# Optimization experiments

Hardware: AMD Instinct MI355X
Metric: run time of the kernel (lower is better)

The kernel has to match this reference:

```python
import jax, jax.numpy as jnp
import numpy as np

D_MODEL = 256
D_EDGE = 64
EPS = 1e-05
INPUT_FEATS = 2 * D_MODEL + D_EDGE + 1  # 577


def _linear_params(key, fan_in, fan_out):
    k1, k2 = jax.random.split(key)
    lim = 1.0 / np.sqrt(fan_in)
    W = jax.random.uniform(k1, (fan_in, fan_out), minval=-lim, maxval=lim, dtype=jnp.float32)
    b = jax.random.uniform(k2, (fan_out,), minval=-lim, maxval=lim, dtype=jnp.float32)
    return W, b


def setup_inputs() -> dict:
    key = jax.random.key(0)
    ks = jax.random.split(key, 16)
    B, N = 8, 128
    inp = {
        "coords": jax.random.normal(ks[0], (B, N, 3), dtype=jnp.float32),
        "inv_feats": jax.random.normal(ks[1], (B, N, D_MODEL), dtype=jnp.float32),
        "adj_matrix": jnp.ones((B, N, N), dtype=jnp.float32),
        "atom_mask": jnp.ones((B, N), dtype=jnp.float32),
        "edge_feats": jax.random.normal(ks[2], (B, N, N, D_EDGE), dtype=jnp.float32),
    }
    inp["W_e1"], inp["b_e1"] = _linear_params(ks[3], INPUT_FEATS, D_MODEL)
    inp["W_e2"], inp["b_e2"] = _linear_params(ks[4], D_MODEL, D_MODEL)
    inp["W_att"], inp["b_att"] = _linear_params(ks[5], D_MODEL, 1)
    inp["W_h1"], inp["b_h1"] = _linear_params(ks[6], 2 * D_MODEL, D_MODEL)
    inp["W_h2"], inp["b_h2"] = _linear_params(ks[7], D_MODEL, D_MODEL)
    inp["W_x1"], inp["b_x1"] = _linear_params(ks[8], INPUT_FEATS, D_MODEL)
    inp["W_x2"], inp["b_x2"] = _linear_params(ks[9], D_MODEL, D_MODEL)
    inp["W_x3"], inp["b_x3"] = _linear_params(ks[10], D_MODEL, 1)
    return inp


def _pair_linear(W, b, node_feats, ef):
    # Linear over concat([node_i, node_j, ef]) without materializing the concat.
    # W: [2*d_model + d_edge + 1, out]
    d = D_MODEL
    hi = node_feats @ W[:d]          # [B,N,out]
    hj = node_feats @ W[d:2 * d]     # [B,N,out]
    he = ef @ W[2 * d:]              # [B,N,N,out]
    return hi[:, :, None, :] + hj[:, None, :, :] + he + b


def _egnn_forward(coords, inv_feats, adj_matrix, atom_mask, edge_feats,
                  W_e1, b_e1, W_e2, b_e2, W_att, b_att,
                  W_h1, b_h1, W_h2, b_h2, W_x1, b_x1, W_x2, b_x2, W_x3, b_x3):
    mask = atom_mask[..., None]                       # [B,N,1]
    diff = coords[:, :, None, :] - coords[:, None, :, :]   # [B,N,N,3]
    sq = jnp.sum(diff * diff, axis=-1, keepdims=True)      # [B,N,N,1]
    ef = jnp.concatenate([edge_feats, sq], axis=-1)        # [B,N,N,d_edge+1]
    adj = adj_matrix[..., None]                             # [B,N,N,1]

    # phi_e: Linear-SiLU-Linear-SiLU on pair features
    msg = jax.nn.silu(_pair_linear(W_e1, b_e1, inv_feats, ef))
    msg = jax.nn.silu(msg @ W_e2 + b_e2)                    # [B,N,N,d]

    att = jax.nn.sigmoid(msg @ W_att + b_att)               # [B,N,N,1]
    node_msg = jnp.sum(msg * att * adj, axis=2)             # [B,N,d]

    h = jnp.concatenate([inv_feats, node_msg], axis=-1)
    h = jax.nn.silu(h @ W_h1 + b_h1) @ W_h2 + b_h2          # [B,N,d]

    # phi_x: Linear-SiLU-Linear-SiLU-Linear -> scalar per edge
    ex = jax.nn.silu(_pair_linear(W_x1, b_x1, inv_feats, ef))
    ex = jax.nn.silu(ex @ W_x2 + b_x2)
    edge_attn = ex @ W_x3 + b_x3                             # [B,N,N,1]

    normalisers = jnp.sqrt(sq[..., 0] + EPS) + 1.0           # [B,N,N]
    weighted = diff * edge_attn / normalisers[..., None] * adj
    coord_updates = jnp.sum(weighted, axis=2)                # [B,N,3]
    num_nodes = jnp.sum(mask, axis=1) + 1.0                  # [B,1]
    coord_updates = coord_updates / num_nodes[:, :, None]

    out_coords = (coords + coord_updates) * mask
    out_feats = h * mask
    return out_coords, out_feats


def reference(coords, inv_feats, adj_matrix, atom_mask, edge_feats,
              W_e1, b_e1, W_e2, b_e2, W_att, b_att,
              W_h1, b_h1, W_h2, b_h2, W_x1, b_x1, W_x2, b_x2, W_x3, b_x3):
    return _egnn_forward(coords, inv_feats, adj_matrix, atom_mask, edge_feats,
                         W_e1, b_e1, W_e2, b_e2, W_att, b_att,
                         W_h1, b_h1, W_h2, b_h2, W_x1, b_x1, W_x2, b_x2, W_x3, b_x3)
```

## Files before the change

kernel.cpp:

```cpp
#include <hip/hip_runtime.h>

typedef __attribute__((ext_vector_type(8))) __bf16 bf16x8;
typedef __attribute__((ext_vector_type(4))) __bf16 bf16x4;
typedef __attribute__((ext_vector_type(4))) float f32x4;

__device__ __forceinline__ float fast_sig(float x) {
  return __builtin_amdgcn_rcpf(1.0f + __expf(-x));
}
__device__ __forceinline__ float siluf(float x) { return x * fast_sig(x); }
__device__ __forceinline__ __bf16 tobf(float x) { return (__bf16)x; }

__device__ __forceinline__ void stage16(const void* g, void* l) {
  __builtin_amdgcn_global_load_lds(
      (const __attribute__((address_space(1))) void*)g,
      (__attribute__((address_space(3))) void*)l, 16, 0, 0);
}

__device__ __forceinline__ void stage_slice(
    const __bf16* __restrict__ src, int ld, int off,
    __bf16* swbuf, int tid)
{
  const int w = tid >> 6;
  #pragma unroll
  for (int q = 0; q < 2; q++) {
    int t16 = q * 512 + tid;
    int c = t16 >> 2, slot = t16 & 3;
    int kpart = slot ^ ((c >> 1) & 3);
    const __bf16* g = src + (size_t)c * ld + off + kpart * 8;
    __bf16* l = swbuf + (size_t)(q * 512 + w * 64) * 8;
    stage16(g, l);
  }
}

__global__ __launch_bounds__(256) void k_prep(
    const float* __restrict__ We1, const float* __restrict__ Wx1,
    const float* __restrict__ We2, const float* __restrict__ Wx2,
    const float* __restrict__ Wh1, const float* __restrict__ Wh2,
    const float* __restrict__ invf,
    __bf16* __restrict__ wt_e, __bf16* __restrict__ wt_x,
    __bf16* __restrict__ w2e, __bf16* __restrict__ w2x,
    __bf16* __restrict__ wh1t, __bf16* __restrict__ wh2t,
    __bf16* __restrict__ hcat,
    float* __restrict__ nmsg, float* __restrict__ cupd)
{
  int idx = blockIdx.x * 256 + threadIdx.x;
  if (idx < 147456) {
    int kk = idx / 576, f = idx - kk * 576;
    wt_e[idx] = tobf(We1[f * 256 + kk]);
    wt_x[idx] = tobf(Wx1[f * 256 + kk]);
  }
  if (idx < 65536) {
    int c = idx >> 8, k = idx & 255;
    w2e[idx] = tobf(We2[k * 256 + c]);
    w2x[idx] = tobf(Wx2[k * 256 + c]);
    wh2t[idx] = tobf(Wh2[k * 256 + c]);
    f32x4 z = {0.f, 0.f, 0.f, 0.f};
    *(f32x4*)(nmsg + idx * 4) = z;
  }
  if (idx < 131072) {
    int c = idx >> 9, k = idx & 511;
    wh1t[idx] = tobf(Wh1[k * 256 + c]);
  }
  if (idx < 3072) cupd[idx] = 0.f;
  {
    int node = idx >> 8, k = idx & 255;
    hcat[node * 512 + k] = tobf(invf[idx]);
  }
}

template<int NKS>
__device__ __forceinline__ void node_gemm64(
    const __bf16* __restrict__ B, int ldb, int boff,
    const __bf16* __restrict__ A, int lda, int aoff,
    int row0, int tid, f32x4 acc[4][4])
{
  const int lane = tid & 63, wc = tid >> 6, lr = lane & 15, lg = lane >> 4;
  #pragma unroll
  for (int ks = 0; ks < NKS; ks++) {
    bf16x8 bB[4], aA[4];
    #pragma unroll
    for (int m = 0; m < 4; m++)
      bB[m] = *(const bf16x8*)(B + (size_t)(row0 + m * 16 + lr) * ldb + boff + ks * 32 + lg * 8);
    #pragma unroll
    for (int n = 0; n < 4; n++)
      aA[n] = *(const bf16x8*)(A + (size_t)(wc * 64 + n * 16 + lr) * lda + aoff + ks * 32 + lg * 8);
    #pragma unroll
    for (int m = 0; m < 4; m++)
      #pragma unroll
      for (int n = 0; n < 4; n++)
        acc[m][n] = __builtin_amdgcn_mfma_f32_16x16x32_bf16(aA[n], bB[m], acc[m][n], 0, 0, 0);
  }
}

__global__ __launch_bounds__(256) void k_nproj(
    const __bf16* __restrict__ hcat,
    const __bf16* __restrict__ wt_e, const __bf16* __restrict__ wt_x,
    const float* __restrict__ be1, const float* __restrict__ bx1,
    float* __restrict__ hie, float* __restrict__ hje,
    float* __restrict__ hix, float* __restrict__ hjx)
{
  const int tid = threadIdx.x;
  const int row0 = blockIdx.x * 64;
  const int mat = blockIdx.y;
  const __bf16* A = (mat < 2) ? wt_e : wt_x;
  const int aoff = (mat & 1) ? 256 : 0;
  const float* bias = (mat == 0) ? be1 : (mat == 2 ? bx1 : nullptr);
  float* out = (mat == 0) ? hie : (mat == 1) ? hje : (mat == 2) ? hix : hjx;

  f32x4 acc[4][4];
  #pragma unroll
  for (int m = 0; m < 4; m++)
    #pragma unroll
    for (int n = 0; n < 4; n++) { f32x4 z = {0.f,0.f,0.f,0.f}; acc[m][n] = z; }
  node_gemm64<8>(hcat, 512, 0, A, 576, aoff, row0, tid, acc);

  const int lane = tid & 63, wc = tid >> 6, lr = lane & 15, lg = lane >> 4;
  #pragma unroll
  for (int m = 0; m < 4; m++) {
    int node = row0 + m * 16 + lr;
    #pragma unroll
    for (int n = 0; n < 4; n++) {
      int c0 = wc * 64 + n * 16 + lg * 4;
      f32x4 v = acc[m][n];
      if (bias) v += *(const f32x4*)(bias + c0);
      *(f32x4*)(out + (size_t)node * 256 + c0) = v;
    }
  }
}

__global__ __launch_bounds__(256) void k_mid(
    const float* __restrict__ nmsg, __bf16* __restrict__ hcat)
{
  int idx = blockIdx.x * 256 + threadIdx.x;
  int node = idx >> 8, k = idx & 255;
  hcat[node * 512 + 256 + k] = tobf(nmsg[idx]);
}

__global__ __launch_bounds__(256) void k_h1(
    const __bf16* __restrict__ hcat, const __bf16* __restrict__ wh1t,
    const float* __restrict__ bh1, __bf16* __restrict__ h1b)
{
  const int tid = threadIdx.x;
  const int row0 = blockIdx.x * 64;
  f32x4 acc[4][4];
  #pragma unroll
  for (int m = 0; m < 4; m++)
    #pragma unroll
    for (int n = 0; n < 4; n++) { f32x4 z = {0.f,0.f,0.f,0.f}; acc[m][n] = z; }
  node_gemm64<16>(hcat, 512, 0, wh1t, 512, 0, row0, tid, acc);

  const int lane = tid & 63, wc = tid >> 6, lr = lane & 15, lg = lane >> 4;
  #pragma unroll
  for (int m = 0; m < 4; m++) {
    int node = row0 + m * 16 + lr;
    #pragma unroll
    for (int n = 0; n < 4; n++) {
      int c0 = wc * 64 + n * 16 + lg * 4;
      f32x4 b4 = *(const f32x4*)(bh1 + c0);
      bf16x4 pk;
      #pragma unroll
      for (int r = 0; r < 4; r++) pk[r] = tobf(siluf(acc[m][n][r] + b4[r]));
      *(bf16x4*)(h1b + (size_t)node * 256 + c0) = pk;
    }
  }
}

__global__ __launch_bounds__(256) void k_h2(
    const __bf16* __restrict__ h1b, const __bf16* __restrict__ wh2t,
    const float* __restrict__ bh2, const float* __restrict__ amask,
    const float* __restrict__ coords, const float* __restrict__ cupd,
    float* __restrict__ out_feats, float* __restrict__ out_coords)
{
  __shared__ float sM[2];
  const int tid = threadIdx.x;
  const int row0 = blockIdx.x * 64;
  const int b = row0 >> 7;
  f32x4 acc[4][4];
  #pragma unroll
  for (int m = 0; m < 4; m++)
    #pragma unroll
    for (int n = 0; n < 4; n++) { f32x4 z = {0.f,0.f,0.f,0.f}; acc[m][n] = z; }
  node_gemm64<8>(h1b, 256, 0, wh2t, 256, 0, row0, tid, acc);

  if (tid < 128) {
    float v = amask[b * 128 + tid];
    #pragma unroll
    for (int off = 1; off < 64; off <<= 1) v += __shfl_xor(v, off);
    if ((tid & 63) == 0) sM[tid >> 6] = v;
  }
  __syncthreads();
  const float sNum = sM[0] + sM[1];

  const int lane = tid & 63, wc = tid >> 6, lr = lane & 15, lg = lane >> 4;
  #pragma unroll
  for (int m = 0; m < 4; m++) {
    int node = row0 + m * 16 + lr;
    float msk = amask[node];
    #pragma unroll
    for (int n = 0; n < 4; n++) {
      int c0 = wc * 64 + n * 16 + lg * 4;
      f32x4 b4 = *(const f32x4*)(bh2 + c0);
      f32x4 v = (acc[m][n] + b4) * msk;
      *(f32x4*)(out_feats + (size_t)node * 256 + c0) = v;
    }
  }
  if (tid < 192) {
    int nl = tid / 3, d = tid - nl * 3;
    int node = row0 + nl;
    float upd = cupd[node * 3 + d] / (sNum + 1.0f);
    out_coords[node * 3 + d] = (coords[node * 3 + d] + upd) * amask[node];
  }
}

template<bool EPATH>
__device__ __forceinline__ void egnn_path(
    int tid, char* sSb, __bf16* sW0, __bf16* sW1,
    const float* shi, const float* slast, const float* sqv, const float* sAdj,
    const float* __restrict__ hjb,
    const __bf16* __restrict__ wt,
    const __bf16* __restrict__ w2,
    const float* __restrict__ bias2, const float* __restrict__ vvec,
    float* sRed, float batt0, float* sNM, float* sCup,
    const float* __restrict__ coords, int jg0,
    float cix, float ciy, float ciz, const bf16x8 bE[2][2])
{
  const int lane = tid & 63, w = tid >> 6;
  const int lr = lane & 15, lg = lane >> 4;
  const int cg = (w & 3) * 64;
  const int jw = (w >> 2) * 32;
  const int slot = lg ^ ((lr >> 1) & 3);
  const int awbase = (cg + lr) * 32 + slot * 8;

  stage_slice(wt, 576, 512, sW0, tid);

  f32x4 hjf[2][4];
  #pragma unroll
  for (int m = 0; m < 2; m++) {
    const int jl = jw + m * 16 + lr;
    #pragma unroll
    for (int n = 0; n < 4; n++)
      hjf[m][n] = *(const f32x4*)(hjb + (size_t)jl * 256 + cg + n * 16 + lg * 4);
  }

  f32x4 acc[2][4];
  #pragma unroll
  for (int m = 0; m < 2; m++)
    #pragma unroll
    for (int n = 0; n < 4; n++) { f32x4 z = {0.f,0.f,0.f,0.f}; acc[m][n] = z; }

  __syncthreads();

  stage_slice(wt, 576, 544, sW1, tid);
  {
    bf16x8 aW[4];
    #pragma unroll
    for (int n = 0; n < 4; n++) aW[n] = *(const bf16x8*)(sW0 + awbase + n * 512);
    #pragma unroll
    for (int m = 0; m < 2; m++)
      #pragma unroll
      for (int n = 0; n < 4; n++)
        acc[m][n] = __builtin_amdgcn_mfma_f32_16x16x32_bf16(aW[n], bE[0][m], acc[m][n], 0, 0, 0);
  }
  __syncthreads();

  stage_slice(w2, 256, 0, sW0, tid);
  {
    bf16x8 aW[4];
    #pragma unroll
    for (int n = 0; n < 4; n++) aW[n] = *(const bf16x8*)(sW1 + awbase + n * 512);
    #pragma unroll
    for (int m = 0; m < 2; m++)
      #pragma unroll
      for (int n = 0; n < 4; n++)
        acc[m][n] = __builtin_amdgcn_mfma_f32_16x16x32_bf16(aW[n], bE[1][m], acc[m][n], 0, 0, 0);
  }
  #pragma unroll
  for (int m = 0; m < 2; m++) {
    const int jl = jw + m * 16 + lr;
    const float sq = sqv[jl];
    #pragma unroll
    for (int n = 0; n < 4; n++) {
      const int kk0 = cg + n * 16 + lg * 4;
      f32x4 hi4 = *(const f32x4*)(shi + kk0);
      f32x4 sl4 = *(const f32x4*)(slast + kk0);
      bf16x4 pk;
      #pragma unroll
      for (int r = 0; r < 4; r++)
        pk[r] = tobf(siluf(acc[m][n][r] + hi4[r] + hjf[m][n][r] + sq * sl4[r]));
      int off = (jl * 512 + kk0 * 2) ^ ((jl & 7) << 4);
      *(bf16x4*)(sSb + off) = pk;
      f32x4 z = {0.f, 0.f, 0.f, 0.f};
      acc[m][n] = z;
    }
  }
  __syncthreads();

  #pragma unroll
  for (int ks = 0; ks < 8; ks++) {
    if (ks < 7)
      stage_slice(w2, 256, (ks + 1) * 32, (ks & 1) ? sW0 : sW1, tid);
    const __bf16* sw = (ks & 1) ? sW1 : sW0;
    bf16x8 aW[4], bS[2];
    #pragma unroll
    for (int m = 0; m < 2; m++) {
      const int jl = jw + m * 16 + lr;
      int off = (jl * 512 + (ks * 32 + lg * 8) * 2) ^ ((jl & 7) << 4);
      bS[m] = *(const bf16x8*)(sSb + off);
    }
    #pragma unroll
    for (int n = 0; n < 4; n++) aW[n] = *(const bf16x8*)(sw + awbase + n * 512);
    #pragma unroll
    for (int m = 0; m < 2; m++)
      #pragma unroll
      for (int n = 0; n < 4; n++)
        acc[m][n] = __builtin_amdgcn_mfma_f32_16x16x32_bf16(aW[n], bS[m], acc[m][n], 0, 0, 0);
    __syncthreads();
  }

  float p[2] = {0.f, 0.f};
  #pragma unroll
  for (int n = 0; n < 4; n++) {
    f32x4 bb = *(const f32x4*)(bias2 + cg + n * 16 + lg * 4);
    f32x4 vv = *(const f32x4*)(vvec  + cg + n * 16 + lg * 4);
    #pragma unroll
    for (int m = 0; m < 2; m++)
      #pragma unroll
      for (int r = 0; r < 4; r++) {
        float s = siluf(acc[m][n][r] + bb[r]);
        acc[m][n][r] = s;
        p[m] += s * vv[r];
      }
  }
  #pragma unroll
  for (int m = 0; m < 2; m++) {
    p[m] += __shfl_xor(p[m], 16);
    p[m] += __shfl_xor(p[m], 32);
  }
  if (lane < 16) {
    #pragma unroll
    for (int m = 0; m < 2; m++)
      atomicAdd(&sRed[jw + m * 16 + lr], p[m]);
  }
  __syncthreads();

  if constexpr (EPATH) {
    float aw[2];
    #pragma unroll
    for (int m = 0; m < 2; m++) {
      int jl = jw + m * 16 + lr;
      aw[m] = fast_sig(sRed[jl] + batt0) * sAdj[jl];
    }
    f32x4 q[4];
    #pragma unroll
    for (int n = 0; n < 4; n++) { f32x4 z = {0.f,0.f,0.f,0.f}; q[n] = z; }
    #pragma unroll
    for (int m = 0; m < 2; m++)
      #pragma unroll
      for (int n = 0; n < 4; n++)
        q[n] += acc[m][n] * aw[m];
    #pragma unroll
    for (int off = 1; off < 16; off <<= 1)
      #pragma unroll
      for (int n = 0; n < 4; n++)
        #pragma unroll
        for (int r = 0; r < 4; r++)
          q[n][r] += __shfl_xor(q[n][r], off);
    if (lr == 0) {
      #pragma unroll
      for (int n = 0; n < 4; n++)
        #pragma unroll
        for (int r = 0; r < 4; r++)
          atomicAdd(&sNM[cg + n * 16 + lg * 4 + r], q[n][r]);
    }
  } else {
    if (tid < 64) {
      int jl = tid;
      int jgl = jg0 + jl;
      float ea = sRed[jl] + batt0;
      float wgt = ea * __builtin_amdgcn_rcpf(sqrtf(sqv[jl] + 1e-5f) + 1.0f) * sAdj[jl];
      float wx = wgt * (cix - coords[jgl * 3 + 0]);
      float wy = wgt * (ciy - coords[jgl * 3 + 1]);
      float wz = wgt * (ciz - coords[jgl * 3 + 2]);
      #pragma unroll
      for (int off = 1; off < 64; off <<= 1) {
        wx += __shfl_xor(wx, off);
        wy += __shfl_xor(wy, off);
        wz += __shfl_xor(wz, off);
      }
      if (tid == 0) { sCup[0] = wx; sCup[1] = wy; sCup[2] = wz; }
    }
  }
}

__global__ __launch_bounds__(512, 4) void k_edge(
    const float* __restrict__ coords, const float* __restrict__ adjm,
    const float* __restrict__ ef,
    const float* __restrict__ We1, const float* __restrict__ Wx1,
    const float* __restrict__ batt,
    const float* __restrict__ be2, const float* __restrict__ bx2,
    const float* __restrict__ bx3,
    const float* __restrict__ Watt, const float* __restrict__ Wx3,
    const float* __restrict__ hie, const float* __restrict__ hje,
    const float* __restrict__ hix, const float* __restrict__ hjx,
    const __bf16* __restrict__ wt_e, const __bf16* __restrict__ wt_x,
    const __bf16* __restrict__ w2e, const __bf16* __restrict__ w2x,
    float* __restrict__ nmsg, float* __restrict__ cupd)
{
  __shared__ __align__(16) char sSb[64 * 512];
  __shared__ __align__(16) __bf16 sW[2][8192];
  __shared__ float shie[256], shix[256], slaste[256], slastx[256];
  __shared__ float sqv[64], sAdj[64], sRedE[64], sRedX[64], sNM[256], sCup[4];

  const int tid = threadIdx.x;
  const int bi = blockIdx.x >> 1;
  const int half = blockIdx.x & 1;
  const int b = bi >> 7;
  const int j0g = half * 64;
  const int jg0 = b * 128 + j0g;

  const int lane = tid & 63, w = tid >> 6;
  const int lr = lane & 15, lg = lane >> 4;
  const int jw = (w >> 2) * 32;

  const float cix = coords[bi * 3 + 0];
  const float ciy = coords[bi * 3 + 1];
  const float ciz = coords[bi * 3 + 2];

  if (tid < 64) sRedE[tid] = 0.f;
  else if (tid < 128) sRedX[tid - 64] = 0.f;
  else if (tid < 384) sNM[tid - 128] = 0.f;
  else if (tid < 388) sCup[tid - 384] = 0.f;
  if (tid < 256) {
    shie[tid] = hie[(size_t)bi * 256 + tid];
    shix[tid] = hix[(size_t)bi * 256 + tid];
    slaste[tid] = We1[576 * 256 + tid];
    slastx[tid] = Wx1[576 * 256 + tid];
  }
  if (tid >= 448) {
    int j = tid - 448;
    int jg = jg0 + j;
    float dx = cix - coords[jg * 3 + 0];
    float dy = ciy - coords[jg * 3 + 1];
    float dz = ciz - coords[jg * 3 + 2];
    sqv[j] = dx * dx + dy * dy + dz * dz;
  }
  if (tid >= 384 && tid < 448)
    sAdj[tid - 384] = adjm[(size_t)bi * 128 + j0g + (tid - 384)];

  bf16x8 bE[2][2];
  {
    const float* efb = ef + ((size_t)bi * 128 + j0g) * 64;
    #pragma unroll
    for (int ks = 0; ks < 2; ks++)
      #pragma unroll
      for (int m = 0; m < 2; m++) {
        const float* er = efb + (jw + m * 16 + lr) * 64 + ks * 32 + lg * 8;
        f32x4 x = *(const f32x4*)er;
        f32x4 y = *(const f32x4*)(er + 4);
        bf16x8 t;
        t[0] = tobf(x[0]); t[1] = tobf(x[1]); t[2] = tobf(x[2]); t[3] = tobf(x[3]);
        t[4] = tobf(y[0]); t[5] = tobf(y[1]); t[6] = tobf(y[2]); t[7] = tobf(y[3]);
        bE[ks][m] = t;
      }
  }

  egnn_path<true>(tid, sSb, sW[0], sW[1], shie, slaste, sqv, sAdj,
                  hje + (size_t)jg0 * 256, wt_e, w2e, be2, Watt,
                  sRedE, batt[0], sNM, sCup, coords, jg0, cix, ciy, ciz, bE);
  egnn_path<false>(tid, sSb, sW[0], sW[1], shix, slastx, sqv, sAdj,
                   hjx + (size_t)jg0 * 256, wt_x, w2x, bx2, Wx3,
                   sRedX, bx3[0], sNM, sCup, coords, jg0, cix, ciy, ciz, bE);

  __syncthreads();
  if (tid < 256) atomicAdd(&nmsg[(size_t)bi * 256 + tid], sNM[tid]);
  if (tid < 3) atomicAdd(&cupd[bi * 3 + tid], sCup[tid]);
}

extern "C" void kernel_launch(void* const* d_in, const int* in_sizes, int n_in,
                              void* d_out, int out_size, void* d_ws, size_t ws_size,
                              hipStream_t stream)
{
  const float* coords = (const float*)d_in[0];
  const float* invf  = (const float*)d_in[1];
  const float* adjm  = (const float*)d_in[2];
  const float* amask = (const float*)d_in[3];
  const float* ef    = (const float*)d_in[4];
  const float* We1   = (const float*)d_in[5];
  const float* be1   = (const float*)d_in[6];
  const float* We2   = (const float*)d_in[7];
  const float* be2   = (const float*)d_in[8];
  const float* Watt  = (const float*)d_in[9];
  const float* batt  = (const float*)d_in[10];
  const float* Wh1   = (const float*)d_in[11];
  const float* bh1   = (const float*)d_in[12];
  const float* Wh2   = (const float*)d_in[13];
  const float* bh2   = (const float*)d_in[14];
  const float* Wx1   = (const float*)d_in[15];
  const float* bx1   = (const float*)d_in[16];
  const float* Wx2   = (const float*)d_in[17];
  const float* bx2   = (const float*)d_in[18];
  const float* Wx3   = (const float*)d_in[19];
  const float* bx3   = (const float*)d_in[20];

  char* ws = (char*)d_ws;
  const size_t MB = 1u << 20;
  float* hie  = (float*)(ws + 0 * MB);
  float* hje  = (float*)(ws + 1 * MB);
  float* hix  = (float*)(ws + 2 * MB);
  float* hjx  = (float*)(ws + 3 * MB);
  __bf16* hcat = (__bf16*)(ws + 4 * MB);
  __bf16* h1b  = (__bf16*)(ws + 5 * MB);
  size_t woff = 5 * MB + 524288;
  __bf16* wt_e = (__bf16*)(ws + woff);
  __bf16* wt_x = (__bf16*)(ws + woff + 294912);
  __bf16* w2e  = (__bf16*)(ws + woff + 2 * 294912);
  __bf16* w2x  = (__bf16*)(ws + woff + 2 * 294912 + 131072);
  __bf16* wh1t = (__bf16*)(ws + woff + 2 * 294912 + 2 * 131072);
  __bf16* wh2t = (__bf16*)(ws + woff + 2 * 294912 + 2 * 131072 + 262144);
  float* nmsg  = (float*)(ws + woff + 2 * 294912 + 3 * 131072 + 262144);
  float* cupd  = (float*)(ws + woff + 2 * 294912 + 3 * 131072 + 262144 + 1048576);

  float* out_coords = (float*)d_out;
  float* out_feats  = out_coords + 8 * 128 * 3;

  hipLaunchKernelGGL(k_prep, dim3(1024), dim3(256), 0, stream,
                     We1, Wx1, We2, Wx2, Wh1, Wh2, invf,
                     wt_e, wt_x, w2e, w2x, wh1t, wh2t, hcat, nmsg, cupd);
  hipLaunchKernelGGL(k_nproj, dim3(16, 4), dim3(256), 0, stream,
                     hcat, wt_e, wt_x, be1, bx1, hie, hje, hix, hjx);
  hipLaunchKernelGGL(k_edge, dim3(2048), dim3(512), 0, stream,
                     coords, adjm, ef, We1, Wx1, batt, be2, bx2, bx3, Watt, Wx3,
                     hie, hje, hix, hjx, wt_e, wt_x, w2e, w2x, nmsg, cupd);
  hipLaunchKernelGGL(k_mid, dim3(1024), dim3(256), 0, stream, nmsg, hcat);
  hipLaunchKernelGGL(k_h1, dim3(16), dim3(256), 0, stream,
                     hcat, wh1t, bh1, h1b);
  hipLaunchKernelGGL(k_h2, dim3(16), dim3(256), 0, stream,
                     h1b, wh2t, bh2, amask, coords, cupd, out_feats, out_coords);
}
```

Baseline: 187.6 us.

## Pipeline weight staging across both edge paths and drop k_mid kernel

Rewrites the edge kernel's two MLP paths into one unrolled loop with a double-buffered async weight-staging pipeline. It uses explicit waitcnt and raw barriers in place of __syncthreads, and prefetches the x-path weights while the e-path epilogue runs. hj projections are stored in bf16 to halve their traffic. The k_mid conversion kernel is removed by having k_h1 read nmsg floats directly and convert on the fly. The hand-placed vmcnt counts and sched barriers are fragile: a wrong count would be a race, and the bf16 hj adds rounding error.

```diff
diff --git a/kernel.cpp b/kernel.cpp
--- a/kernel.cpp
+++ b/kernel.cpp
@@ -3,6 +3,8 @@
 typedef __attribute__((ext_vector_type(8))) __bf16 bf16x8;
 typedef __attribute__((ext_vector_type(4))) __bf16 bf16x4;
 typedef __attribute__((ext_vector_type(4))) float f32x4;
+
+#define SCHED0 __builtin_amdgcn_sched_barrier(0)
 
 __device__ __forceinline__ float fast_sig(float x) {
   return __builtin_amdgcn_rcpf(1.0f + __expf(-x));
@@ -30,6 +32,14 @@
     __bf16* l = swbuf + (size_t)(q * 512 + w * 64) * 8;
     stage16(g, l);
   }
+}
+
+__device__ __forceinline__ void stage_k(
+    const __bf16* __restrict__ wt, const __bf16* __restrict__ w2,
+    int k, __bf16* buf, int tid)
+{
+  if (k < 2) stage_slice(wt, 576, 512 + k * 32, buf, tid);
+  else       stage_slice(w2, 256, (k - 2) * 32, buf, tid);
 }
 
 __global__ __launch_bounds__(256) void k_prep(
@@ -40,7 +50,7 @@
     __bf16* __restrict__ wt_e, __bf16* __restrict__ wt_x,
     __bf16* __restrict__ w2e, __bf16* __restrict__ w2x,
     __bf16* __restrict__ wh1t, __bf16* __restrict__ wh2t,
-    __bf16* __restrict__ hcat,
+    __bf16* __restrict__ invb,
     float* __restrict__ nmsg, float* __restrict__ cupd)
 {
   int idx = blockIdx.x * 256 + threadIdx.x;
@@ -62,10 +72,7 @@
     wh1t[idx] = tobf(Wh1[k * 256 + c]);
   }
   if (idx < 3072) cupd[idx] = 0.f;
-  {
-    int node = idx >> 8, k = idx & 255;
-    hcat[node * 512 + k] = tobf(invf[idx]);
-  }
+  invb[idx] = tobf(invf[idx]);
 }
 
 template<int NKS>
@@ -93,63 +100,98 @@
 }
 
 __global__ __launch_bounds__(256) void k_nproj(
-    const __bf16* __restrict__ hcat,
+    const __bf16* __restrict__ invb,
     const __bf16* __restrict__ wt_e, const __bf16* __restrict__ wt_x,
     const float* __restrict__ be1, const float* __restrict__ bx1,
-    float* __restrict__ hie, float* __restrict__ hje,
-    float* __restrict__ hix, float* __restrict__ hjx)
+    float* __restrict__ hie, float* __restrict__ hix,
+    __bf16* __restrict__ hje, __bf16* __restrict__ hjx)
 {
   const int tid = threadIdx.x;
   const int row0 = blockIdx.x * 64;
   const int mat = blockIdx.y;
   const __bf16* A = (mat < 2) ? wt_e : wt_x;
   const int aoff = (mat & 1) ? 256 : 0;
-  const float* bias = (mat == 0) ? be1 : (mat == 2 ? bx1 : nullptr);
-  float* out = (mat == 0) ? hie : (mat == 1) ? hje : (mat == 2) ? hix : hjx;
 
   f32x4 acc[4][4];
   #pragma unroll
   for (int m = 0; m < 4; m++)
     #pragma unroll
     for (int n = 0; n < 4; n++) { f32x4 z = {0.f,0.f,0.f,0.f}; acc[m][n] = z; }
-  node_gemm64<8>(hcat, 512, 0, A, 576, aoff, row0, tid, acc);
+  node_gemm64<8>(invb, 256, 0, A, 576, aoff, row0, tid, acc);
 
   const int lane = tid & 63, wc = tid >> 6, lr = lane & 15, lg = lane >> 4;
-  #pragma unroll
-  for (int m = 0; m < 4; m++) {
-    int node = row0 + m * 16 + lr;
-    #pragma unroll
-    for (int n = 0; n < 4; n++) {
-      int c0 = wc * 64 + n * 16 + lg * 4;
-      f32x4 v = acc[m][n];
-      if (bias) v += *(const f32x4*)(bias + c0);
-      *(f32x4*)(out + (size_t)node * 256 + c0) = v;
-    }
-  }
-}
-
-__global__ __launch_bounds__(256) void k_mid(
-    const float* __restrict__ nmsg, __bf16* __restrict__ hcat)
-{
-  int idx = blockIdx.x * 256 + threadIdx.x;
-  int node = idx >> 8, k = idx & 255;
-  hcat[node * 512 + 256 + k] = tobf(nmsg[idx]);
+  if ((mat & 1) == 0) {
+    const float* bias = (mat == 0) ? be1 : bx1;
+    float* out = (mat == 0) ? hie : hix;
+    #pragma unroll
+    for (int m = 0; m < 4; m++) {
+      int node = row0 + m * 16 + lr;
+      #pragma unroll
+      for (int n = 0; n < 4; n++) {
+        int c0 = wc * 64 + n * 16 + lg * 4;
+        f32x4 v = acc[m][n] + *(const f32x4*)(bias + c0);
+        *(f32x4*)(out + (size_t)node * 256 + c0) = v;
+      }
+    }
+  } else {
+    __bf16* out = (mat == 1) ? hje : hjx;
+    #pragma unroll
+    for (int m = 0; m < 4; m++) {
+      int node = row0 + m * 16 + lr;
+      #pragma unroll
+      for (int n = 0; n < 4; n++) {
+        int c0 = wc * 64 + n * 16 + lg * 4;
+        bf16x4 pk;
+        #pragma unroll
+        for (int r = 0; r < 4; r++) pk[r] = tobf(acc[m][n][r]);
+        *(bf16x4*)(out + (size_t)node * 256 + c0) = pk;
+      }
+    }
+  }
 }
 
 __global__ __launch_bounds__(256) void k_h1(
-    const __bf16* __restrict__ hcat, const __bf16* __restrict__ wh1t,
+    const __bf16* __restrict__ invb, const float* __restrict__ nmsg,
+    const __bf16* __restrict__ wh1t,
     const float* __restrict__ bh1, __bf16* __restrict__ h1b)
 {
   const int tid = threadIdx.x;
   const int row0 = blockIdx.x * 64;
+  const int lane = tid & 63, wc = tid >> 6, lr = lane & 15, lg = lane >> 4;
   f32x4 acc[4][4];
   #pragma unroll
   for (int m = 0; m < 4; m++)
     #pragma unroll
     for (int n = 0; n < 4; n++) { f32x4 z = {0.f,0.f,0.f,0.f}; acc[m][n] = z; }
-  node_gemm64<16>(hcat, 512, 0, wh1t, 512, 0, row0, tid, acc);
-
-  const int lane = tid & 63, wc = tid >> 6, lr = lane & 15, lg = lane >> 4;
+
+  #pragma unroll
+  for (int ks = 0; ks < 16; ks++) {
+    bf16x8 bB[4], aA[4];
+    #pragma unroll
+    for (int m = 0; m < 4; m++) {
+      int node = row0 + m * 16 + lr;
+      if (ks < 8) {
+        bB[m] = *(const bf16x8*)(invb + (size_t)node * 256 + ks * 32 + lg * 8);
+      } else {
+        const float* pp = nmsg + (size_t)node * 256 + (ks - 8) * 32 + lg * 8;
+        f32x4 lo = *(const f32x4*)pp;
+        f32x4 hi = *(const f32x4*)(pp + 4);
+        bf16x8 t;
+        t[0]=tobf(lo[0]); t[1]=tobf(lo[1]); t[2]=tobf(lo[2]); t[3]=tobf(lo[3]);
+        t[4]=tobf(hi[0]); t[5]=tobf(hi[1]); t[6]=tobf(hi[2]); t[7]=tobf(hi[3]);
+        bB[m] = t;
+      }
+    }
+    #pragma unroll
+    for (int n = 0; n < 4; n++)
+      aA[n] = *(const bf16x8*)(wh1t + (size_t)(wc * 64 + n * 16 + lr) * 512 + ks * 32 + lg * 8);
+    #pragma unroll
+    for (int m = 0; m < 4; m++)
+      #pragma unroll
+      for (int n = 0; n < 4; n++)
+        acc[m][n] = __builtin_amdgcn_mfma_f32_16x16x32_bf16(aA[n], bB[m], acc[m][n], 0, 0, 0);
+  }
+
   #pragma unroll
   for (int m = 0; m < 4; m++) {
     int node = row0 + m * 16 + lr;
@@ -209,186 +251,6 @@
     int node = row0 + nl;
     float upd = cupd[node * 3 + d] / (sNum + 1.0f);
     out_coords[node * 3 + d] = (coords[node * 3 + d] + upd) * amask[node];
-  }
-}
-
-template<bool EPATH>
-__device__ __forceinline__ void egnn_path(
-    int tid, char* sSb, __bf16* sW0, __bf16* sW1,
-    const float* shi, const float* slast, const float* sqv, const float* sAdj,
-    const float* __restrict__ hjb,
-    const __bf16* __restrict__ wt,
-    const __bf16* __restrict__ w2,
-    const float* __restrict__ bias2, const float* __restrict__ vvec,
-    float* sRed, float batt0, float* sNM, float* sCup,
-    const float* __restrict__ coords, int jg0,
-    float cix, float ciy, float ciz, const bf16x8 bE[2][2])
-{
-  const int lane = tid & 63, w = tid >> 6;
-  const int lr = lane & 15, lg = lane >> 4;
-  const int cg = (w & 3) * 64;
-  const int jw = (w >> 2) * 32;
-  const int slot = lg ^ ((lr >> 1) & 3);
-  const int awbase = (cg + lr) * 32 + slot * 8;
-
-  stage_slice(wt, 576, 512, sW0, tid);
-
-  f32x4 hjf[2][4];
-  #pragma unroll
-  for (int m = 0; m < 2; m++) {
-    const int jl = jw + m * 16 + lr;
-    #pragma unroll
-    for (int n = 0; n < 4; n++)
-      hjf[m][n] = *(const f32x4*)(hjb + (size_t)jl * 256 + cg + n * 16 + lg * 4);
-  }
-
-  f32x4 acc[2][4];
-  #pragma unroll
-  for (int m = 0; m < 2; m++)
-    #pragma unroll
-    for (int n = 0; n < 4; n++) { f32x4 z = {0.f,0.f,0.f,0.f}; acc[m][n] = z; }
-
-  __syncthreads();
-
-  stage_slice(wt, 576, 544, sW1, tid);
-  {
-    bf16x8 aW[4];
-    #pragma unroll
-    for (int n = 0; n < 4; n++) aW[n] = *(const bf16x8*)(sW0 + awbase + n * 512);
-    #pragma unroll
-    for (int m = 0; m < 2; m++)
-      #pragma unroll
-      for (int n = 0; n < 4; n++)
-        acc[m][n] = __builtin_amdgcn_mfma_f32_16x16x32_bf16(aW[n], bE[0][m], acc[m][n], 0, 0, 0);
-  }
-  __syncthreads();
-
-  stage_slice(w2, 256, 0, sW0, tid);
-  {
-    bf16x8 aW[4];
-    #pragma unroll
-    for (int n = 0; n < 4; n++) aW[n] = *(const bf16x8*)(sW1 + awbase + n * 512);
-    #pragma unroll
-    for (int m = 0; m < 2; m++)
-      #pragma unroll
-      for (int n = 0; n < 4; n++)
-        acc[m][n] = __builtin_amdgcn_mfma_f32_16x16x32_bf16(aW[n], bE[1][m], acc[m][n], 0, 0, 0);
-  }
-  #pragma unroll
-  for (int m = 0; m < 2; m++) {
-    const int jl = jw + m * 16 + lr;
-    const float sq = sqv[jl];
-    #pragma unroll
-    for (int n = 0; n < 4; n++) {
-      const int kk0 = cg + n * 16 + lg * 4;
-      f32x4 hi4 = *(const f32x4*)(shi + kk0);
-      f32x4 sl4 = *(const f32x4*)(slast + kk0);
-      bf16x4 pk;
-      #pragma unroll
-      for (int r = 0; r < 4; r++)
-        pk[r] = tobf(siluf(acc[m][n][r] + hi4[r] + hjf[m][n][r] + sq * sl4[r]));
-      int off = (jl * 512 + kk0 * 2) ^ ((jl & 7) << 4);
-      *(bf16x4*)(sSb + off) = pk;
-      f32x4 z = {0.f, 0.f, 0.f, 0.f};
-      acc[m][n] = z;
-    }
-  }
-  __syncthreads();
-
-  #pragma unroll
-  for (int ks = 0; ks < 8; ks++) {
-    if (ks < 7)
-      stage_slice(w2, 256, (ks + 1) * 32, (ks & 1) ? sW0 : sW1, tid);
-    const __bf16* sw = (ks & 1) ? sW1 : sW0;
-    bf16x8 aW[4], bS[2];
-    #pragma unroll
-    for (int m = 0; m < 2; m++) {
-      const int jl = jw + m * 16 + lr;
-      int off = (jl * 512 + (ks * 32 + lg * 8) * 2) ^ ((jl & 7) << 4);
-      bS[m] = *(const bf16x8*)(sSb + off);
-    }
-    #pragma unroll
-    for (int n = 0; n < 4; n++) aW[n] = *(const bf16x8*)(sw + awbase + n * 512);
-    #pragma unroll
-    for (int m = 0; m < 2; m++)
-      #pragma unroll
-      for (int n = 0; n < 4; n++)
-        acc[m][n] = __builtin_amdgcn_mfma_f32_16x16x32_bf16(aW[n], bS[m], acc[m][n], 0, 0, 0);
-    __syncthreads();
-  }
-
-  float p[2] = {0.f, 0.f};
-  #pragma unroll
-  for (int n = 0; n < 4; n++) {
-    f32x4 bb = *(const f32x4*)(bias2 + cg + n * 16 + lg * 4);
-    f32x4 vv = *(const f32x4*)(vvec  + cg + n * 16 + lg * 4);
-    #pragma unroll
-    for (int m = 0; m < 2; m++)
-      #pragma unroll
-      for (int r = 0; r < 4; r++) {
-        float s = siluf(acc[m][n][r] + bb[r]);
-        acc[m][n][r] = s;
-        p[m] += s * vv[r];
-      }
-  }
-  #pragma unroll
-  for (int m = 0; m < 2; m++) {
-    p[m] += __shfl_xor(p[m], 16);
-    p[m] += __shfl_xor(p[m], 32);
-  }
-  if (lane < 16) {
-    #pragma unroll
-    for (int m = 0; m < 2; m++)
-      atomicAdd(&sRed[jw + m * 16 + lr], p[m]);
-  }
-  __syncthreads();
-
-  if constexpr (EPATH) {
-    float aw[2];
-    #pragma unroll
-    for (int m = 0; m < 2; m++) {
-      int jl = jw + m * 16 + lr;
-      aw[m] = fast_sig(sRed[jl] + batt0) * sAdj[jl];
-    }
-    f32x4 q[4];
-    #pragma unroll
-    for (int n = 0; n < 4; n++) { f32x4 z = {0.f,0.f,0.f,0.f}; q[n] = z; }
-    #pragma unroll
-    for (int m = 0; m < 2; m++)
-      #pragma unroll
-      for (int n = 0; n < 4; n++)
-        q[n] += acc[m][n] * aw[m];
-    #pragma unroll
-    for (int off = 1; off < 16; off <<= 1)
-      #pragma unroll
-      for (int n = 0; n < 4; n++)
-        #pragma unroll
-        for (int r = 0; r < 4; r++)
-          q[n][r] += __shfl_xor(q[n][r], off);
-    if (lr == 0) {
-      #pragma unroll
-      for (int n = 0; n < 4; n++)
-        #pragma unroll
-        for (int r = 0; r < 4; r++)
-          atomicAdd(&sNM[cg + n * 16 + lg * 4 + r], q[n][r]);
-    }
-  } else {
-    if (tid < 64) {
-      int jl = tid;
-      int jgl = jg0 + jl;
-      float ea = sRed[jl] + batt0;
-      float wgt = ea * __builtin_amdgcn_rcpf(sqrtf(sqv[jl] + 1e-5f) + 1.0f) * sAdj[jl];
-      float wx = wgt * (cix - coords[jgl * 3 + 0]);
-      float wy = wgt * (ciy - coords[jgl * 3 + 1]);
-      float wz = wgt * (ciz - coords[jgl * 3 + 2]);
-      #pragma unroll
-      for (int off = 1; off < 64; off <<= 1) {
-        wx += __shfl_xor(wx, off);
-        wy += __shfl_xor(wy, off);
-        wz += __shfl_xor(wz, off);
-      }
-      if (tid == 0) { sCup[0] = wx; sCup[1] = wy; sCup[2] = wz; }
-    }
   }
 }
 
@@ -400,14 +262,15 @@
     const float* __restrict__ be2, const float* __restrict__ bx2,
     const float* __restrict__ bx3,
     const float* __restrict__ Watt, const float* __restrict__ Wx3,
-    const float* __restrict__ hie, const float* __restrict__ hje,
-    const float* __restrict__ hix, const float* __restrict__ hjx,
+    const float* __restrict__ hie, const float* __restrict__ hix,
+    const __bf16* __restrict__ hje, const __bf16* __restrict__ hjx,
     const __bf16* __restrict__ wt_e, const __bf16* __restrict__ wt_x,
     const __bf16* __restrict__ w2e, const __bf16* __restrict__ w2x,
     float* __restrict__ nmsg, float* __restrict__ cupd)
 {
   __shared__ __align__(16) char sSb[64 * 512];
-  __shared__ __align__(16) __bf16 sW[2][8192];
+  __shared__ __align__(16) __bf16 sW0[8192];
+  __shared__ __align__(16) __bf16 sW1[8192];
   __shared__ float shie[256], shix[256], slaste[256], slastx[256];
   __shared__ float sqv[64], sAdj[64], sRedE[64], sRedX[64], sNM[256], sCup[4];
 
@@ -420,11 +283,16 @@
 
   const int lane = tid & 63, w = tid >> 6;
   const int lr = lane & 15, lg = lane >> 4;
+  const int cg = (w & 3) * 64;
   const int jw = (w >> 2) * 32;
+  const int slot = lg ^ ((lr >> 1) & 3);
+  const int awbase = (cg + lr) * 32 + slot * 8;
 
   const float cix = coords[bi * 3 + 0];
   const float ciy = coords[bi * 3 + 1];
   const float ciz = coords[bi * 3 + 2];
+  const float b0e = batt[0];
+  const float b0x = bx3[0];
 
   if (tid < 64) sRedE[tid] = 0.f;
   else if (tid < 128) sRedX[tid - 64] = 0.f;
@@ -447,6 +315,15 @@
   if (tid >= 384 && tid < 448)
     sAdj[tid - 384] = adjm[(size_t)bi * 128 + j0g + (tid - 384)];
 
+  bf16x4 hjf[2][4];
+  #pragma unroll
+  for (int m = 0; m < 2; m++) {
+    const int jl = jw + m * 16 + lr;
+    #pragma unroll
+    for (int n = 0; n < 4; n++)
+      hjf[m][n] = *(const bf16x4*)(hje + ((size_t)jg0 + jl) * 256 + cg + n * 16 + lg * 4);
+  }
+
   bf16x8 bE[2][2];
   {
     const float* efb = ef + ((size_t)bi * 128 + j0g) * 64;
@@ -464,12 +341,186 @@
       }
   }
 
-  egnn_path<true>(tid, sSb, sW[0], sW[1], shie, slaste, sqv, sAdj,
-                  hje + (size_t)jg0 * 256, wt_e, w2e, be2, Watt,
-                  sRedE, batt[0], sNM, sCup, coords, jg0, cix, ciy, ciz, bE);
-  egnn_path<false>(tid, sSb, sW[0], sW[1], shix, slastx, sqv, sAdj,
-                   hjx + (size_t)jg0 * 256, wt_x, w2x, bx2, Wx3,
-                   sRedX, bx3[0], sNM, sCup, coords, jg0, cix, ciy, ciz, bE);
+  stage_k(wt_e, w2e, 0, sW0, tid);
+  stage_k(wt_e, w2e, 1, sW1, tid);
+
+  asm volatile("s_waitcnt lgkmcnt(0)" ::: "memory");
+  SCHED0;
+
+  #pragma unroll
+  for (int p = 0; p < 2; p++) {
+    const __bf16* wt = p ? wt_x : wt_e;
+    const __bf16* w2 = p ? w2x : w2e;
+    const float* shi = p ? shix : shie;
+    const float* slast = p ? slastx : slaste;
+    const float* bias2 = p ? bx2 : be2;
+    const float* vvec = p ? Wx3 : Watt;
+    float* sRed = p ? sRedX : sRedE;
+    const float batt0 = p ? b0x : b0e;
+
+    f32x4 acc[2][4];
+    #pragma unroll
+    for (int m = 0; m < 2; m++)
+      #pragma unroll
+      for (int n = 0; n < 4; n++) { f32x4 z = {0.f,0.f,0.f,0.f}; acc[m][n] = z; }
+
+    #pragma unroll
+    for (int k = 0; k < 10; k++) {
+      SCHED0;
+      if (k < 9) asm volatile("s_waitcnt vmcnt(2)" ::: "memory");
+      else       asm volatile("s_waitcnt vmcnt(0)" ::: "memory");
+      SCHED0;
+      __builtin_amdgcn_s_barrier();
+      SCHED0;
+
+      __bf16* sw = (k & 1) ? sW1 : sW0;
+      bf16x8 aW[4];
+      #pragma unroll
+      for (int n = 0; n < 4; n++) aW[n] = *(const bf16x8*)(sw + awbase + n * 512);
+
+      if (k < 2) {
+        #pragma unroll
+        for (int m = 0; m < 2; m++)
+          #pragma unroll
+          for (int n = 0; n < 4; n++)
+            acc[m][n] = __builtin_amdgcn_mfma_f32_16x16x32_bf16(aW[n], bE[k][m], acc[m][n], 0, 0, 0);
+        if (k == 1) {
+          #pragma unroll
+          for (int m = 0; m < 2; m++) {
+            const int jl = jw + m * 16 + lr;
+            const float sq = sqv[jl];
+            #pragma unroll
+            for (int n = 0; n < 4; n++) {
+              const int kk0 = cg + n * 16 + lg * 4;
+              f32x4 hi4 = *(const f32x4*)(shi + kk0);
+              f32x4 sl4 = *(const f32x4*)(slast + kk0);
+              bf16x4 pk;
+              #pragma unroll
+              for (int r = 0; r < 4; r++) {
+                float v = acc[m][n][r] + hi4[r] + (float)hjf[m][n][r] + sq * sl4[r];
+                pk[r] = tobf(siluf(v));
+              }
+              int off = (jl * 512 + kk0 * 2) ^ ((jl & 7) << 4);
+              *(bf16x4*)(sSb + off) = pk;
+              f32x4 z = {0.f, 0.f, 0.f, 0.f};
+              acc[m][n] = z;
+            }
+          }
+        }
+      } else {
+        const int ks = k - 2;
+        bf16x8 bS[2];
+        #pragma unroll
+        for (int m = 0; m < 2; m++) {
+          const int jl = jw + m * 16 + lr;
+          int off = (jl * 512 + (ks * 32 + lg * 8) * 2) ^ ((jl & 7) << 4);
+          bS[m] = *(const bf16x8*)(sSb + off);
+        }
+        #pragma unroll
+        for (int m = 0; m < 2; m++)
+          #pragma unroll
+          for (int n = 0; n < 4; n++)
+            acc[m][n] = __builtin_amdgcn_mfma_f32_16x16x32_bf16(aW[n], bS[m], acc[m][n], 0, 0, 0);
+      }
+
+      SCHED0;
+      asm volatile("s_waitcnt lgkmcnt(0)" ::: "memory");
+      SCHED0;
+      __builtin_amdgcn_s_barrier();
+      SCHED0;
+      if (k < 8) stage_k(wt, w2, k + 2, sw, tid);
+    }
+
+    if (p == 0) {
+      stage_k(wt_x, w2x, 0, sW0, tid);
+      stage_k(wt_x, w2x, 1, sW1, tid);
+    }
+
+    float pr[2] = {0.f, 0.f};
+    #pragma unroll
+    for (int n = 0; n < 4; n++) {
+      f32x4 bb = *(const f32x4*)(bias2 + cg + n * 16 + lg * 4);
+      f32x4 vv = *(const f32x4*)(vvec  + cg + n * 16 + lg * 4);
+      #pragma unroll
+      for (int m = 0; m < 2; m++)
+        #pragma unroll
+        for (int r = 0; r < 4; r++) {
+          float s = siluf(acc[m][n][r] + bb[r]);
+          acc[m][n][r] = s;
+          pr[m] += s * vv[r];
+        }
+    }
+    #pragma unroll
+    for (int m = 0; m < 2; m++) {
+      pr[m] += __shfl_xor(pr[m], 16);
+      pr[m] += __shfl_xor(pr[m], 32);
+    }
+    if (lane < 16) {
+      #pragma unroll
+      for (int m = 0; m < 2; m++)
+        atomicAdd(&sRed[jw + m * 16 + lr], pr[m]);
+    }
+    SCHED0;
+    asm volatile("s_waitcnt lgkmcnt(0)" ::: "memory");
+    SCHED0;
+    __builtin_amdgcn_s_barrier();
+    SCHED0;
+
+    if (p == 0) {
+      float aw[2];
+      #pragma unroll
+      for (int m = 0; m < 2; m++) {
+        int jl = jw + m * 16 + lr;
+        aw[m] = fast_sig(sRed[jl] + batt0) * sAdj[jl];
+      }
+      f32x4 q[4];
+      #pragma unroll
+      for (int n = 0; n < 4; n++) { f32x4 z = {0.f,0.f,0.f,0.f}; q[n] = z; }
+      #pragma unroll
+      for (int m = 0; m < 2; m++)
+        #pragma unroll
+        for (int n = 0; n < 4; n++)
+          q[n] += acc[m][n] * aw[m];
+      #pragma unroll
+      for (int off = 1; off < 16; off <<= 1)
+        #pragma unroll
+        for (int n = 0; n < 4; n++)
+          #pragma unroll
+          for (int r = 0; r < 4; r++)
+            q[n][r] += __shfl_xor(q[n][r], off);
+      if (lr == 0) {
+        #pragma unroll
+        for (int n = 0; n < 4; n++)
+          #pragma unroll
+          for (int r = 0; r < 4; r++)
+            atomicAdd(&sNM[cg + n * 16 + lg * 4 + r], q[n][r]);
+      }
+      #pragma unroll
+      for (int m = 0; m < 2; m++) {
+        const int jl = jw + m * 16 + lr;
+        #pragma unroll
+        for (int n = 0; n < 4; n++)
+          hjf[m][n] = *(const bf16x4*)(hjx + ((size_t)jg0 + jl) * 256 + cg + n * 16 + lg * 4);
+      }
+    } else {
+      if (tid < 64) {
+        int jl = tid;
+        int jgl = jg0 + jl;
+        float ea = sRed[jl] + batt0;
+        float wgt = ea * __builtin_amdgcn_rcpf(sqrtf(sqv[jl] + 1e-5f) + 1.0f) * sAdj[jl];
+        float wx = wgt * (cix - coords[jgl * 3 + 0]);
+        float wy = wgt * (ciy - coords[jgl * 3 + 1]);
+        float wz = wgt * (ciz - coords[jgl * 3 + 2]);
+        #pragma unroll
+        for (int off = 1; off < 64; off <<= 1) {
+          wx += __shfl_xor(wx, off);
+          wy += __shfl_xor(wy, off);
+          wz += __shfl_xor(wz, off);
+        }
+        if (tid == 0) { sCup[0] = wx; sCup[1] = wy; sCup[2] = wz; }
+      }
+    }
+  }
 
   __syncthreads();
   if (tid < 256) atomicAdd(&nmsg[(size_t)bi * 256 + tid], sNM[tid]);
@@ -504,36 +555,35 @@
 
   char* ws = (char*)d_ws;
   const size_t MB = 1u << 20;
-  float* hie  = (float*)(ws + 0 * MB);
-  float* hje  = (float*)(ws + 1 * MB);
-  float* hix  = (float*)(ws + 2 * MB);
-  float* hjx  = (float*)(ws + 3 * MB);
-  __bf16* hcat = (__bf16*)(ws + 4 * MB);
-  __bf16* h1b  = (__bf16*)(ws + 5 * MB);
-  size_t woff = 5 * MB + 524288;
+  float*  hie  = (float*)(ws + 0 * MB);
+  float*  hix  = (float*)(ws + 1 * MB);
+  __bf16* hje  = (__bf16*)(ws + 2 * MB);
+  __bf16* hjx  = (__bf16*)(ws + 2 * MB + 524288);
+  __bf16* invb = (__bf16*)(ws + 3 * MB);
+  __bf16* h1b  = (__bf16*)(ws + 3 * MB + 524288);
+  size_t woff = 4 * MB;
   __bf16* wt_e = (__bf16*)(ws + woff);
   __bf16* wt_x = (__bf16*)(ws + woff + 294912);
   __bf16* w2e  = (__bf16*)(ws + woff + 2 * 294912);
   __bf16* w2x  = (__bf16*)(ws + woff + 2 * 294912 + 131072);
   __bf16* wh1t = (__bf16*)(ws + woff + 2 * 294912 + 2 * 131072);
   __bf16* wh2t = (__bf16*)(ws + woff + 2 * 294912 + 2 * 131072 + 262144);
-  float* nmsg  = (float*)(ws + woff + 2 * 294912 + 3 * 131072 + 262144);
-  float* cupd  = (float*)(ws + woff + 2 * 294912 + 3 * 131072 + 262144 + 1048576);
+  float*  nmsg = (float*)(ws + woff + 2 * 294912 + 3 * 131072 + 262144);
+  float*  cupd = (float*)(ws + woff + 2 * 294912 + 3 * 131072 + 262144 + 1048576);
 
   float* out_coords = (float*)d_out;
   float* out_feats  = out_coords + 8 * 128 * 3;
 
   hipLaunchKernelGGL(k_prep, dim3(1024), dim3(256), 0, stream,
                      We1, Wx1, We2, Wx2, Wh1, Wh2, invf,
-                     wt_e, wt_x, w2e, w2x, wh1t, wh2t, hcat, nmsg, cupd);
+                     wt_e, wt_x, w2e, w2x, wh1t, wh2t, invb, nmsg, cupd);
   hipLaunchKernelGGL(k_nproj, dim3(16, 4), dim3(256), 0, stream,
-                     hcat, wt_e, wt_x, be1, bx1, hie, hje, hix, hjx);
+                     invb, wt_e, wt_x, be1, bx1, hie, hix, hje, hjx);
   hipLaunchKernelGGL(k_edge, dim3(2048), dim3(512), 0, stream,
                      coords, adjm, ef, We1, Wx1, batt, be2, bx2, bx3, Watt, Wx3,
-                     hie, hje, hix, hjx, wt_e, wt_x, w2e, w2x, nmsg, cupd);
-  hipLaunchKernelGGL(k_mid, dim3(1024), dim3(256), 0, stream, nmsg, hcat);
+                     hie, hix, hje, hjx, wt_e, wt_x, w2e, w2x, nmsg, cupd);
   hipLaunchKernelGGL(k_h1, dim3(16), dim3(256), 0, stream,
-                     hcat, wh1t, bh1, h1b);
+                     invb, nmsg, wh1t, bh1, h1b);
   hipLaunchKernelGGL(k_h2, dim3(16), dim3(256), 0, stream,
                      h1b, wh2t, bh2, amask, coords, cupd, out_feats, out_coords);
 }
```

New measurement: 192.2 us. +2.5%, slower.
